# Performance work log

Measured on AMD Instinct MI355X. Metric: run time of the kernel, lower is better.

## Reference

```python
import jax, jax.numpy as jnp
import numpy as np

N_NODES = 50000
N_EDGES = 800000
NODE_DIM = 64
EDGE_DIM = 32
HIDDEN = 128
OUT_DIM = 32
N_LAYERS = 3
NUM_GRAPHS = 128


def setup_inputs() -> dict:
    key = jax.random.key(0)
    ks = jax.random.split(key, 20)
    s = 0.05
    inp = {
        "x": jax.random.normal(ks[0], (N_NODES, NODE_DIM), dtype=jnp.float32),
        "edge_attr": jax.random.normal(ks[1], (N_EDGES, EDGE_DIM), dtype=jnp.float32),
        "edge_index": jax.random.randint(ks[2], (2, N_EDGES), 0, N_NODES, dtype=jnp.int32),
        "batch": jnp.sort(jax.random.randint(ks[3], (N_NODES,), 0, NUM_GRAPHS, dtype=jnp.int32)),
        # per-interaction params, stacked on leading layer axis
        "W_dense": jax.random.normal(ks[4], (N_LAYERS, NODE_DIM, NODE_DIM)) * s,
        "filt_W1": jax.random.normal(ks[5], (N_LAYERS, EDGE_DIM, HIDDEN)) * s,
        "filt_b1": jnp.zeros((N_LAYERS, HIDDEN)),
        "filt_W2": jax.random.normal(ks[6], (N_LAYERS, HIDDEN, NODE_DIM)) * s,
        "filt_b2": jnp.zeros((N_LAYERS, NODE_DIM)),
        "attn_v": jax.random.normal(ks[7], (N_LAYERS, NODE_DIM)) * s,
        "out_W1": jax.random.normal(ks[8], (N_LAYERS, NODE_DIM, HIDDEN)) * s,
        "out_b1": jnp.zeros((N_LAYERS, HIDDEN)),
        "out_W2": jax.random.normal(ks[9], (N_LAYERS, HIDDEN, NODE_DIM)) * s,
        "out_b2": jnp.zeros((N_LAYERS, NODE_DIM)),
        # output network
        "net_W1": jax.random.normal(ks[10], (NODE_DIM, HIDDEN)) * s,
        "net_b1": jnp.zeros((HIDDEN,)),
        "net_W2": jax.random.normal(ks[11], (HIDDEN, OUT_DIM)) * s,
        "net_b2": jnp.zeros((OUT_DIM,)),
    }
    return inp


def _mlp2(x, W1, b1, W2, b2):
    # 2-layer MLP with tanh after first layer (matches MLP(num_layers=2, act='tanh'))
    return jnp.tanh(x @ W1 + b1) @ W2 + b2


def reference(x, edge_attr, W_dense, filt_W1, filt_b1, filt_W2, filt_b2,
              attn_v, out_W1, out_b1, out_W2, out_b2,
              net_W1, net_b1, net_W2, net_b2, edge_index, batch):
    n_nodes = x.shape[0]
    src, tgt = edge_index[0], edge_index[1]
    h = x
    for i in range(N_LAYERS):
        hd = h @ W_dense[i]                                   # initial_dense (no bias)
        edge_w = _mlp2(edge_attr, filt_W1[i], filt_b1[i], filt_W2[i], filt_b2[i])  # [E, D]
        messages = hd[src] * edge_w                           # [E, D]
        # per-target segment softmax over attention scores
        scores = messages @ attn_v[i]                         # [E]
        seg_max = jax.ops.segment_max(scores, tgt, num_segments=n_nodes)
        exp_s = jnp.exp(scores - seg_max[tgt])
        denom = jax.ops.segment_sum(exp_s, tgt, num_segments=n_nodes)
        attn_w = exp_s / denom[tgt]                           # [E]
        messages = messages * attn_w[:, None]
        agg = jax.ops.segment_sum(messages, tgt, num_segments=n_nodes)  # [N, D]
        delta = _mlp2(agg, out_W1[i], out_b1[i], out_W2[i], out_b2[i])
        h = h + delta                                         # residual
    # mean pooling per graph
    pooled = jax.ops.segment_sum(h, batch, num_segments=NUM_GRAPHS)
    counts = jnp.bincount(batch, length=NUM_GRAPHS)
    pooled = pooled / jnp.maximum(counts, 1)[:, None].astype(h.dtype)
    out = _mlp2(pooled, net_W1, net_b1, net_W2, net_b2)       # [G, OUT_DIM]
    return out
```

## Files before the change

### kernel.cpp

```cpp
#include <hip/hip_runtime.h>
#include <hip/hip_bf16.h>
#include <math.h>

#define NODE_DIM 64
#define EDGE_DIM 32
#define HIDDEN   128
#define OUT_DIM  32
#define N_LAYERS 3
#define NGRAPH   128

typedef __attribute__((ext_vector_type(8))) short bf16x8;
typedef __attribute__((ext_vector_type(4))) float f32x4;

__device__ __forceinline__ unsigned short f2bf(float f) {
    unsigned u = __float_as_uint(f);
    u = (u + 0x7fffu + ((u >> 16) & 1u)) >> 16;
    return (unsigned short)u;
}
__device__ __forceinline__ float bf2f(unsigned short h) {
    return __uint_as_float((unsigned)h << 16);
}
__device__ __forceinline__ float fast_tanh(float x) {
    float ax = fabsf(x);
    float e = __expf(-2.f * ax);
    float r = __builtin_amdgcn_rcpf(1.f + e);
    float t = (1.f - e) * r;
    return __builtin_copysignf(t, x);
}

__global__ __launch_bounds__(256) void coarse_hist_kernel(
    const int* __restrict__ tgt, int* __restrict__ Hc, int E, int C, int NB) {
    __shared__ int lh[512];
    int blk = blockIdx.x, tid = threadIdx.x;
    for (int b = tid; b < C; b += 256) lh[b] = 0;
    __syncthreads();
    int base = blk * 4096;
#pragma unroll
    for (int i = 0; i < 16; ++i) {
        int e = base + i * 256 + tid;
        if (e < E) atomicAdd(&lh[tgt[e] >> 7], 1);
    }
    __syncthreads();
    for (int b = tid; b < C; b += 256) Hc[(size_t)b * NB + blk] = lh[b];
}

__global__ __launch_bounds__(256) void scan1_kernel(const int* __restrict__ c,
                                                    int* __restrict__ o,
                                                    int* __restrict__ bsum, int n) {
    __shared__ int sh[256];
    int b = blockIdx.x, t = threadIdx.x;
    int i = b * 256 + t;
    int v = (i < n) ? c[i] : 0;
    sh[t] = v;
    __syncthreads();
    for (int d = 1; d < 256; d <<= 1) {
        int u = (t >= d) ? sh[t - d] : 0;
        __syncthreads();
        sh[t] += u;
        __syncthreads();
    }
    if (i < n) o[i] = sh[t] - v;
    if (t == 255) bsum[b] = sh[255];
}

__global__ void scan2_kernel(int* __restrict__ bsum, int nb) {
    __shared__ int sh[1024];
    int t = threadIdx.x;
    int v = (t < nb) ? bsum[t] : 0;
    sh[t] = v;
    __syncthreads();
    for (int d = 1; d < 1024; d <<= 1) {
        int u = (t >= d) ? sh[t - d] : 0;
        __syncthreads();
        sh[t] += u;
        __syncthreads();
    }
    if (t < nb) bsum[t] = sh[t] - v;
}

__global__ __launch_bounds__(256) void scan3_kernel(int* __restrict__ o,
                                                    const int* __restrict__ bsum, int n) {
    int i = blockIdx.x * 256 + threadIdx.x;
    if (i < n) o[i] += bsum[blockIdx.x];
}

__global__ __launch_bounds__(256) void coarse_scatter_kernel(
    const int* __restrict__ tgt, const int* __restrict__ Sc,
    int* __restrict__ tgtc, int* __restrict__ ec, int E, int C, int NB) {
    __shared__ int lb[512];
    int blk = blockIdx.x, tid = threadIdx.x;
    for (int b = tid; b < C; b += 256) lb[b] = Sc[(size_t)b * NB + blk];
    __syncthreads();
    int base = blk * 4096;
#pragma unroll
    for (int i = 0; i < 16; ++i) {
        int e = base + i * 256 + tid;
        if (e < E) {
            int t = tgt[e];
            int pos = atomicAdd(&lb[t >> 7], 1);
            tgtc[pos] = t;
            ec[pos] = e;
        }
    }
}

__global__ __launch_bounds__(256) void fine_sort_kernel(
    const int* __restrict__ Sc, const int* __restrict__ tgtc,
    const int* __restrict__ ec, const int* __restrict__ src,
    int* __restrict__ off, int* __restrict__ eidx, int* __restrict__ srcp,
    int E, int N, int C, int NB) {
    __shared__ int fh[128], fs[128], rb[128];
    int b = blockIdx.x, tid = threadIdx.x;
    int cb0 = Sc[(size_t)b * NB];
    int cb1 = (b + 1 < C) ? Sc[(size_t)(b + 1) * NB] : E;
    if (tid < 128) fh[tid] = 0;
    __syncthreads();
    for (int p = cb0 + tid; p < cb1; p += 256) atomicAdd(&fh[tgtc[p] & 127], 1);
    __syncthreads();
    if (tid < 128) fs[tid] = fh[tid];
    __syncthreads();
    for (int d = 1; d < 128; d <<= 1) {
        int v = 0;
        if (tid < 128 && tid >= d) v = fs[tid - d];
        __syncthreads();
        if (tid < 128) fs[tid] += v;
        __syncthreads();
    }
    if (tid < 128) {
        int ex = fs[tid] - fh[tid];
        rb[tid] = ex;
        int node = (b << 7) + tid;
        if (node < N) off[node] = cb0 + ex;
    }
    if (b == C - 1 && tid == 0) off[N] = E;
    __syncthreads();
    for (int p = cb0 + tid; p < cb1; p += 256) {
        int t = tgtc[p];
        int r = atomicAdd(&rb[t & 127], 1);
        int fpos = cb0 + r;
        int e = ec[p];
        eidx[fpos] = e;
        srcp[fpos] = src[e];
    }
}

__global__ void gbound_kernel(const int* __restrict__ batch, int* __restrict__ goff,
                              int N, int G) {
    int i = blockIdx.x * 256 + threadIdx.x;
    if (i >= N) return;
    int b = batch[i];
    if (i == 0) {
        for (int g = 0; g <= b; ++g) goff[g] = 0;
    } else {
        int bp = batch[i - 1];
        for (int g = bp + 1; g <= b; ++g) goff[g] = i;
    }
    if (i == N - 1) {
        for (int g = b + 1; g <= G; ++g) goff[g] = N;
    }
}

__global__ __launch_bounds__(256) void perm_ea_kernel(
    const float* __restrict__ ea, const int* __restrict__ eidx,
    unsigned short* __restrict__ out, int E) {
    int p = blockIdx.x * 256 + threadIdx.x;
    if (p >= E) return;
    int e = eidx[p];
    const float4* r = (const float4*)(ea + (size_t)e * EDGE_DIM);
    union { unsigned short us[EDGE_DIM]; uint4 u4[EDGE_DIM / 8]; } tmp;
#pragma unroll
    for (int q = 0; q < EDGE_DIM / 4; ++q) {
        float4 v = r[q];
        tmp.us[4 * q]     = f2bf(v.x);
        tmp.us[4 * q + 1] = f2bf(v.y);
        tmp.us[4 * q + 2] = f2bf(v.z);
        tmp.us[4 * q + 3] = f2bf(v.w);
    }
    uint4* o = (uint4*)(out + (size_t)p * EDGE_DIM);
#pragma unroll
    for (int k = 0; k < EDGE_DIM / 8; ++k) o[k] = tmp.u4[k];
}

__global__ void swizzle_w_kernel(const float* __restrict__ fW1, const float* __restrict__ fW2,
                                 const float* __restrict__ oW1, const float* __restrict__ oW2,
                                 unsigned short* __restrict__ W1sw, unsigned short* __restrict__ W2sw,
                                 unsigned short* __restrict__ oW1sw, unsigned short* __restrict__ oW2sw) {
    int i = blockIdx.x / 56, r = blockIdx.x % 56;
    int L = threadIdx.x;
    int e = L & 15, q = L >> 4;
    const float* W;
    unsigned short* out;
    int K, M, t;
    if (r < 8)       { W = fW1 + (size_t)i * EDGE_DIM * HIDDEN;  out = W1sw  + (size_t)i * 8 * 512;  K = EDGE_DIM; M = HIDDEN;   t = r; }
    else if (r < 24) { W = fW2 + (size_t)i * HIDDEN * NODE_DIM;  out = W2sw  + (size_t)i * 16 * 512; K = HIDDEN;   M = NODE_DIM; t = r - 8; }
    else if (r < 40) { W = oW1 + (size_t)i * NODE_DIM * HIDDEN;  out = oW1sw + (size_t)i * 16 * 512; K = NODE_DIM; M = HIDDEN;   t = r - 24; }
    else             { W = oW2 + (size_t)i * HIDDEN * NODE_DIM;  out = oW2sw + (size_t)i * 16 * 512; K = HIDDEN;   M = NODE_DIM; t = r - 40; }
    int nc = K >> 5;
    int mt = t / nc, s = t - mt * nc;
    union { unsigned short us[8]; uint4 u4; } pk;
#pragma unroll
    for (int j = 0; j < 8; ++j)
        pk.us[j] = f2bf(W[(size_t)(32 * s + 8 * q + j) * M + 16 * mt + e]);
    *(uint4*)(out + ((size_t)t * 64 + L) * 8) = pk.u4;
}

#define HSTRIDE 136

__global__ __launch_bounds__(256) void edge_mfma_kernel(
    const unsigned short* __restrict__ ea_p, const float* __restrict__ hd,
    const unsigned short* __restrict__ W1sw, const float* __restrict__ b1,
    const unsigned short* __restrict__ W2sw, const float* __restrict__ b2,
    const float* __restrict__ av, const int* __restrict__ srcp,
    unsigned short* __restrict__ ew, float* __restrict__ score, int E) {
    __shared__ unsigned short Hl[4][16 * HSTRIDE];
    int wave = threadIdx.x >> 6, lane = threadIdx.x & 63;
    int e = lane & 15, q = lane >> 4;
    int p0 = blockIdx.x * 64 + wave * 16;
    if (p0 >= E) return;

    bf16x8 eaf = *(const bf16x8*)(ea_p + (size_t)(p0 + e) * EDGE_DIM + q * 8);

    f32x4 c1[8];
#pragma unroll
    for (int t = 0; t < 8; ++t) {
        bf16x8 a = *(const bf16x8*)(W1sw + (t * 64 + lane) * 8);
        c1[t] = __builtin_amdgcn_mfma_f32_16x16x32_bf16(a, eaf, (f32x4){0.f, 0.f, 0.f, 0.f}, 0, 0, 0);
    }

    unsigned short* hrow = &Hl[wave][e * HSTRIDE];
#pragma unroll
    for (int t = 0; t < 8; ++t) {
        float4 b = *(const float4*)(b1 + 16 * t + 4 * q);
        unsigned h0 = f2bf(fast_tanh(c1[t][0] + b.x));
        unsigned h1 = f2bf(fast_tanh(c1[t][1] + b.y));
        unsigned h2 = f2bf(fast_tanh(c1[t][2] + b.z));
        unsigned h3 = f2bf(fast_tanh(c1[t][3] + b.w));
        uint2 pk;
        pk.x = h0 | (h1 << 16);
        pk.y = h2 | (h3 << 16);
        *(uint2*)(hrow + 16 * t + 4 * q) = pk;
    }

    f32x4 c2[4] = {{0.f, 0.f, 0.f, 0.f}, {0.f, 0.f, 0.f, 0.f},
                   {0.f, 0.f, 0.f, 0.f}, {0.f, 0.f, 0.f, 0.f}};
#pragma unroll
    for (int s = 0; s < 4; ++s) {
        bf16x8 hf = *(const bf16x8*)(hrow + 32 * s + 8 * q);
#pragma unroll
        for (int nt = 0; nt < 4; ++nt) {
            bf16x8 a = *(const bf16x8*)(W2sw + ((nt * 4 + s) * 64 + lane) * 8);
            c2[nt] = __builtin_amdgcn_mfma_f32_16x16x32_bf16(a, hf, c2[nt], 0, 0, 0);
        }
    }

    int sidx = srcp[p0 + e];
    float sc = 0.f;
#pragma unroll
    for (int nt = 0; nt < 4; ++nt) {
        float4 bb = *(const float4*)(b2 + 16 * nt + 4 * q);
        float4 vv = *(const float4*)(av + 16 * nt + 4 * q);
        float4 hh = *(const float4*)(hd + (size_t)sidx * NODE_DIM + 16 * nt + 4 * q);
        float e0 = c2[nt][0] + bb.x, e1 = c2[nt][1] + bb.y;
        float e2 = c2[nt][2] + bb.z, e3 = c2[nt][3] + bb.w;
        uint2 pk;
        pk.x = (unsigned)f2bf(e0) | ((unsigned)f2bf(e1) << 16);
        pk.y = (unsigned)f2bf(e2) | ((unsigned)f2bf(e3) << 16);
        *(uint2*)(ew + (size_t)(p0 + e) * NODE_DIM + 16 * nt + 4 * q) = pk;
        sc += hh.x * e0 * vv.x + hh.y * e1 * vv.y + hh.z * e2 * vv.z + hh.w * e3 * vv.w;
    }
    sc += __shfl_xor(sc, 16, 64);
    sc += __shfl_xor(sc, 32, 64);
    if (q == 0) score[p0 + e] = sc;
}

__global__ __launch_bounds__(256) void node_mlp_kernel(
    const float* __restrict__ agg,
    const unsigned short* __restrict__ W1sw, const float* __restrict__ b1,
    const unsigned short* __restrict__ W2sw, const float* __restrict__ b2,
    float* __restrict__ h, int N) {
    __shared__ unsigned short Hl[4][16 * HSTRIDE];
    int wave = threadIdx.x >> 6, lane = threadIdx.x & 63;
    int e = lane & 15, q = lane >> 4;
    int n0 = (blockIdx.x * 4 + wave) * 16;
    if (n0 >= N) return;
    int ne = n0 + e;
    int neC = ne < N ? ne : N - 1;
    bool ok = ne < N;

    bf16x8 bfr[2];
#pragma unroll
    for (int s = 0; s < 2; ++s) {
        const float4* ar = (const float4*)(agg + (size_t)neC * NODE_DIM + 32 * s + 8 * q);
        float4 x0 = ar[0], x1 = ar[1];
        union { bf16x8 v; unsigned short us[8]; } u;
        u.us[0] = f2bf(x0.x); u.us[1] = f2bf(x0.y);
        u.us[2] = f2bf(x0.z); u.us[3] = f2bf(x0.w);
        u.us[4] = f2bf(x1.x); u.us[5] = f2bf(x1.y);
        u.us[6] = f2bf(x1.z); u.us[7] = f2bf(x1.w);
        bfr[s] = u.v;
    }

    f32x4 c1[8];
#pragma unroll
    for (int t = 0; t < 8; ++t) {
        bf16x8 a0 = *(const bf16x8*)(W1sw + ((t * 2 + 0) * 64 + lane) * 8);
        bf16x8 a1 = *(const bf16x8*)(W1sw + ((t * 2 + 1) * 64 + lane) * 8);
        c1[t] = __builtin_amdgcn_mfma_f32_16x16x32_bf16(a0, bfr[0], (f32x4){0.f, 0.f, 0.f, 0.f}, 0, 0, 0);
        c1[t] = __builtin_amdgcn_mfma_f32_16x16x32_bf16(a1, bfr[1], c1[t], 0, 0, 0);
    }

    unsigned short* hrow = &Hl[wave][e * HSTRIDE];
#pragma unroll
    for (int t = 0; t < 8; ++t) {
        float4 b = *(const float4*)(b1 + 16 * t + 4 * q);
        unsigned h0 = f2bf(fast_tanh(c1[t][0] + b.x));
        unsigned h1 = f2bf(fast_tanh(c1[t][1] + b.y));
        unsigned h2 = f2bf(fast_tanh(c1[t][2] + b.z));
        unsigned h3 = f2bf(fast_tanh(c1[t][3] + b.w));
        uint2 pk;
        pk.x = h0 | (h1 << 16);
        pk.y = h2 | (h3 << 16);
        *(uint2*)(hrow + 16 * t + 4 * q) = pk;
    }

    f32x4 c2[4] = {{0.f, 0.f, 0.f, 0.f}, {0.f, 0.f, 0.f, 0.f},
                   {0.f, 0.f, 0.f, 0.f}, {0.f, 0.f, 0.f, 0.f}};
#pragma unroll
    for (int s = 0; s < 4; ++s) {
        bf16x8 hf = *(const bf16x8*)(hrow + 32 * s + 8 * q);
#pragma unroll
        for (int nt = 0; nt < 4; ++nt) {
            bf16x8 a = *(const bf16x8*)(W2sw + ((nt * 4 + s) * 64 + lane) * 8);
            c2[nt] = __builtin_amdgcn_mfma_f32_16x16x32_bf16(a, hf, c2[nt], 0, 0, 0);
        }
    }

    if (ok) {
#pragma unroll
        for (int nt = 0; nt < 4; ++nt) {
            float4 bb = *(const float4*)(b2 + 16 * nt + 4 * q);
            float4* hp = (float4*)(h + (size_t)ne * NODE_DIM + 16 * nt + 4 * q);
            float4 hv = *hp;
            hv.x += c2[nt][0] + bb.x;
            hv.y += c2[nt][1] + bb.y;
            hv.z += c2[nt][2] + bb.z;
            hv.w += c2[nt][3] + bb.w;
            *hp = hv;
        }
    }
}

template <int K, int M, bool ACT, bool RESID>
__global__ __launch_bounds__(256) void dense_kernel(
    const float* __restrict__ X, const float* __restrict__ W,
    const float* __restrict__ bias, float* __restrict__ Y, int rows) {
    int tid = blockIdx.x * 256 + threadIdx.x;
    int row = tid / M;
    int d = tid - row * M;
    if (row >= rows) return;
    if (M >= 64) row = __builtin_amdgcn_readfirstlane(row);
    const float* __restrict__ x = X + (size_t)row * K;
    float acc = bias ? bias[d] : 0.f;
#pragma unroll
    for (int k = 0; k < K; ++k) acc += x[k] * W[k * M + d];
    if (ACT) acc = fast_tanh(acc);
    if (RESID) acc += Y[(size_t)row * M + d];
    Y[(size_t)row * M + d] = acc;
}

__global__ __launch_bounds__(256) void agg_kernel(
    const unsigned short* __restrict__ ew, const float* __restrict__ score,
    const float* __restrict__ hd, const int* __restrict__ srcp,
    const int* __restrict__ off, float* __restrict__ agg, int n) {
    int tid = blockIdx.x * 256 + threadIdx.x;
    int wid = tid >> 6;
    int lane = threadIdx.x & 63;
    if (wid >= n) return;
    wid = __builtin_amdgcn_readfirstlane(wid);
    int o0 = off[wid], o1 = off[wid + 1];
    int g = lane >> 3, s = lane & 7;
    if (o1 <= o0) {
        if (g == 0) {
            float4 z = {0.f, 0.f, 0.f, 0.f};
            float4* dst = (float4*)(agg + (size_t)wid * NODE_DIM + s * 8);
            dst[0] = z; dst[1] = z;
        }
        return;
    }
    float m = -INFINITY;
    for (int p = o0 + lane; p < o1; p += 64) m = fmaxf(m, score[p]);
#pragma unroll
    for (int t = 32; t; t >>= 1) m = fmaxf(m, __shfl_xor(m, t, 64));
    float dsum = 0.f;
    for (int p = o0 + lane; p < o1; p += 64) dsum += __expf(score[p] - m);
#pragma unroll
    for (int t = 32; t; t >>= 1) dsum += __shfl_xor(dsum, t, 64);

    float acc[8] = {0.f, 0.f, 0.f, 0.f, 0.f, 0.f, 0.f, 0.f};
    for (int p = o0; p < o1; p += 8) {
        int pe = p + g;
        int pc = (pe < o1) ? pe : (o1 - 1);
        float w = (pe < o1) ? __expf(score[pc] - m) : 0.f;
        int sidx = srcp[pc];
        union { bf16x8 v; unsigned short us[8]; } eu;
        eu.v = *(const bf16x8*)(ew + (size_t)pc * NODE_DIM + s * 8);
        const float4* hr = (const float4*)(hd + (size_t)sidx * NODE_DIM + s * 8);
        float4 h0 = hr[0], h1 = hr[1];
        acc[0] += w * h0.x * bf2f(eu.us[0]);
        acc[1] += w * h0.y * bf2f(eu.us[1]);
        acc[2] += w * h0.z * bf2f(eu.us[2]);
        acc[3] += w * h0.w * bf2f(eu.us[3]);
        acc[4] += w * h1.x * bf2f(eu.us[4]);
        acc[5] += w * h1.y * bf2f(eu.us[5]);
        acc[6] += w * h1.z * bf2f(eu.us[6]);
        acc[7] += w * h1.w * bf2f(eu.us[7]);
    }
#pragma unroll
    for (int j = 0; j < 8; ++j) {
        acc[j] += __shfl_xor(acc[j], 8, 64);
        acc[j] += __shfl_xor(acc[j], 16, 64);
        acc[j] += __shfl_xor(acc[j], 32, 64);
    }
    if (g == 0) {
        float inv = __builtin_amdgcn_rcpf(dsum);
        inv = inv * (2.f - dsum * inv);
        float4 r0 = {acc[0] * inv, acc[1] * inv, acc[2] * inv, acc[3] * inv};
        float4 r1 = {acc[4] * inv, acc[5] * inv, acc[6] * inv, acc[7] * inv};
        float4* dst = (float4*)(agg + (size_t)wid * NODE_DIM + s * 8);
        dst[0] = r0; dst[1] = r1;
    }
}

__global__ __launch_bounds__(256) void pool_kernel(const float* __restrict__ h,
                                                   const int* __restrict__ goff,
                                                   float* __restrict__ pooled) {
    __shared__ float sh[4][NODE_DIM];
    int g = blockIdx.x;
    int w = threadIdx.x >> 6, d = threadIdx.x & 63;
    int o0 = goff[g], o1 = goff[g + 1];
    float acc = 0.f;
    for (int n = o0 + w; n < o1; n += 4) acc += h[(size_t)n * NODE_DIM + d];
    sh[w][d] = acc;
    __syncthreads();
    if (w == 0) {
        float sum = sh[0][d] + sh[1][d] + sh[2][d] + sh[3][d];
        int c = o1 - o0;
        if (c < 1) c = 1;
        pooled[g * NODE_DIM + d] = sum / (float)c;
    }
}

extern "C" void kernel_launch(void* const* d_in, const int* in_sizes, int n_in,
                              void* d_out, int out_size, void* d_ws, size_t ws_size,
                              hipStream_t stream) {
    const float* x         = (const float*)d_in[0];
    const float* edge_attr = (const float*)d_in[1];
    const int*   ei        = (const int*)d_in[2];
    const int*   batch     = (const int*)d_in[3];
    const float* Wd        = (const float*)d_in[4];
    const float* fW1       = (const float*)d_in[5];
    const float* fb1       = (const float*)d_in[6];
    const float* fW2       = (const float*)d_in[7];
    const float* fb2       = (const float*)d_in[8];
    const float* av        = (const float*)d_in[9];
    const float* oW1       = (const float*)d_in[10];
    const float* ob1       = (const float*)d_in[11];
    const float* oW2       = (const float*)d_in[12];
    const float* ob2       = (const float*)d_in[13];
    const float* nW1       = (const float*)d_in[14];
    const float* nb1       = (const float*)d_in[15];
    const float* nW2       = (const float*)d_in[16];
    const float* nb2       = (const float*)d_in[17];
    float* out = (float*)d_out;

    const int N = in_sizes[0] / NODE_DIM;
    const int E = in_sizes[2] / 2;
    const int G = NGRAPH;
    const int NB = (E + 4095) / 4096;
    const int C  = (N + 127) >> 7;
    const int SN = C * NB;
    const int SB = (SN + 255) / 256;

    char* base = (char*)d_ws;
    size_t pos = 0;
    auto alloc = [&](size_t bytes) -> void* {
        pos = (pos + 255) & ~(size_t)255;
        void* r = base + pos;
        pos += bytes;
        return r;
    };
    int* Hc   = (int*)alloc((size_t)SN * 4);
    int* Sc   = (int*)alloc(((size_t)SN + 1) * 4);
    int* bsum = (int*)alloc((size_t)1024 * 4);
    int* tgtc = (int*)alloc((size_t)E * 4);
    int* ec   = (int*)alloc((size_t)E * 4);
    int* off  = (int*)alloc((size_t)(N + 1) * 4);
    int* goff = (int*)alloc((size_t)(G + 1) * 4);
    int* eidx = (int*)alloc((size_t)E * 4);
    int* srcp = (int*)alloc((size_t)E * 4);
    float* score = (float*)alloc((size_t)E * 4);
    float* hd    = (float*)alloc((size_t)N * NODE_DIM * 4);
    float* h     = (float*)alloc((size_t)N * NODE_DIM * 4);
    float* agg   = (float*)alloc((size_t)N * NODE_DIM * 4);
    float* pooled = (float*)alloc((size_t)G * NODE_DIM * 4);
    float* t2     = (float*)alloc((size_t)G * HIDDEN * 4);
    unsigned short* ea_p  = (unsigned short*)alloc((size_t)E * EDGE_DIM * 2);
    unsigned short* ew    = (unsigned short*)alloc((size_t)E * NODE_DIM * 2);
    unsigned short* W1sw  = (unsigned short*)alloc((size_t)N_LAYERS * 8 * 512 * 2);
    unsigned short* W2sw  = (unsigned short*)alloc((size_t)N_LAYERS * 16 * 512 * 2);
    unsigned short* oW1sw = (unsigned short*)alloc((size_t)N_LAYERS * 16 * 512 * 2);
    unsigned short* oW2sw = (unsigned short*)alloc((size_t)N_LAYERS * 16 * 512 * 2);
    (void)ws_size;

    const int* src = ei;
    const int* tgt = ei + E;

    coarse_hist_kernel<<<NB, 256, 0, stream>>>(tgt, Hc, E, C, NB);
    scan1_kernel<<<SB, 256, 0, stream>>>(Hc, Sc, bsum, SN);
    scan2_kernel<<<1, 1024, 0, stream>>>(bsum, SB);
    scan3_kernel<<<SB, 256, 0, stream>>>(Sc, bsum, SN);
    coarse_scatter_kernel<<<NB, 256, 0, stream>>>(tgt, Sc, tgtc, ec, E, C, NB);
    fine_sort_kernel<<<C, 256, 0, stream>>>(Sc, tgtc, ec, src, off, eidx, srcp, E, N, C, NB);
    gbound_kernel<<<(N + 255) / 256, 256, 0, stream>>>(batch, goff, N, G);
    perm_ea_kernel<<<(E + 255) / 256, 256, 0, stream>>>(edge_attr, eidx, ea_p, E);
    swizzle_w_kernel<<<N_LAYERS * 56, 64, 0, stream>>>(fW1, fW2, oW1, oW2, W1sw, W2sw, oW1sw, oW2sw);
    hipMemcpyAsync(h, x, (size_t)N * NODE_DIM * 4, hipMemcpyDeviceToDevice, stream);

    const int node_tiles = (N + 15) / 16;
    for (int i = 0; i < N_LAYERS; ++i) {
        dense_kernel<NODE_DIM, NODE_DIM, false, false>
            <<<(N * NODE_DIM + 255) / 256, 256, 0, stream>>>(
                h, Wd + (size_t)i * NODE_DIM * NODE_DIM, nullptr, hd, N);
        edge_mfma_kernel<<<(E + 63) / 64, 256, 0, stream>>>(
            ea_p, hd,
            W1sw + (size_t)i * 8 * 512, fb1 + (size_t)i * HIDDEN,
            W2sw + (size_t)i * 16 * 512, fb2 + (size_t)i * NODE_DIM,
            av + (size_t)i * NODE_DIM, srcp, ew, score, E);
        agg_kernel<<<(N + 3) / 4, 256, 0, stream>>>(ew, score, hd, srcp, off, agg, N);
        node_mlp_kernel<<<(node_tiles + 3) / 4, 256, 0, stream>>>(
            agg,
            oW1sw + (size_t)i * 16 * 512, ob1 + (size_t)i * HIDDEN,
            oW2sw + (size_t)i * 16 * 512, ob2 + (size_t)i * NODE_DIM,
            h, N);
    }

    pool_kernel<<<G, 256, 0, stream>>>(h, goff, pooled);
    dense_kernel<NODE_DIM, HIDDEN, true, false>
        <<<(G * HIDDEN + 255) / 256, 256, 0, stream>>>(pooled, nW1, nb1, t2, G);
    dense_kernel<HIDDEN, OUT_DIM, false, false>
        <<<(G * OUT_DIM + 255) / 256, 256, 0, stream>>>(t2, nW2, nb2, out, G);
}
```

Measured before the change: 853.8 us.

## Fuse edge filter MLP, softmax aggregation and node MLP into one per-node-block kernel

Replaces the separate edge MLP, aggregation and node MLP kernels with one kernel. Each block owns 64 target nodes, computes the filter MLP for their CSR-sorted edges, accumulates exp-weighted messages into shared memory with LDS atomics, then runs the output MLP and residual update in place. This removes the global round trips for the bf16 edge weights, the scores and the agg buffer. The softmax no longer subtracts a per-segment max and instead clamps scores at 60, which could lose precision. Load balance now depends on per-block edge counts, and the LDS atomics may contend.

```diff
diff --git a/kernel.cpp b/kernel.cpp
--- a/kernel.cpp
+++ b/kernel.cpp
@@ -108,7 +108,7 @@
     const int* __restrict__ Sc, const int* __restrict__ tgtc,
     const int* __restrict__ ec, const int* __restrict__ src,
     int* __restrict__ off, int* __restrict__ eidx, int* __restrict__ srcp,
-    int E, int N, int C, int NB) {
+    int* __restrict__ tgts, int E, int N, int C, int NB) {
     __shared__ int fh[128], fs[128], rb[128];
     int b = blockIdx.x, tid = threadIdx.x;
     int cb0 = Sc[(size_t)b * NB];
@@ -141,6 +141,7 @@
         int e = ec[p];
         eidx[fpos] = e;
         srcp[fpos] = src[e];
+        tgts[fpos] = t;
     }
 }
 
@@ -205,147 +206,177 @@
 }
 
 #define HSTRIDE 136
-
-__global__ __launch_bounds__(256) void edge_mfma_kernel(
+#define NG 64
+
+__global__ __launch_bounds__(256, 4) void edge_agg_kernel(
     const unsigned short* __restrict__ ea_p, const float* __restrict__ hd,
     const unsigned short* __restrict__ W1sw, const float* __restrict__ b1,
     const unsigned short* __restrict__ W2sw, const float* __restrict__ b2,
     const float* __restrict__ av, const int* __restrict__ srcp,
-    unsigned short* __restrict__ ew, float* __restrict__ score, int E) {
-    __shared__ unsigned short Hl[4][16 * HSTRIDE];
-    int wave = threadIdx.x >> 6, lane = threadIdx.x & 63;
+    const int* __restrict__ tgts, const int* __restrict__ off,
+    const unsigned short* __restrict__ oW1sw, const float* __restrict__ ob1,
+    const unsigned short* __restrict__ oW2sw, const float* __restrict__ ob2,
+    float* __restrict__ h, int N) {
+    __shared__ float scr[4][16 * 68];
+    __shared__ float acc[NG * 65];
+    __shared__ float den[NG];
+
+    int tid = threadIdx.x;
+    int wave = tid >> 6, lane = tid & 63;
     int e = lane & 15, q = lane >> 4;
-    int p0 = blockIdx.x * 64 + wave * 16;
-    if (p0 >= E) return;
-
-    bf16x8 eaf = *(const bf16x8*)(ea_p + (size_t)(p0 + e) * EDGE_DIM + q * 8);
-
-    f32x4 c1[8];
+    int n0 = blockIdx.x * NG;
+    int n1 = n0 + NG; if (n1 > N) n1 = N;
+    int e0 = off[n0], e1 = off[n1];
+
+    for (int i = tid; i < NG * 65; i += 256) acc[i] = 0.f;
+    if (tid < NG) den[tid] = 0.f;
+    __syncthreads();
+
+    float* swrow = &scr[wave][0];
+    unsigned short* hrow = (unsigned short*)swrow + e * HSTRIDE;
+
+    int nch = (e1 - e0 + 63) >> 6;
+    for (int c = 0; c < nch; ++c) {
+        int p0 = e0 + c * 64 + wave * 16;
+        if (p0 < e1) {
+            int pe = p0 + e;
+            int pc = pe < e1 ? pe : e1 - 1;
+            bool valid = pe < e1;
+
+            bf16x8 eaf = *(const bf16x8*)(ea_p + (size_t)pc * EDGE_DIM + q * 8);
+            f32x4 c1[8];
+#pragma unroll
+            for (int t = 0; t < 8; ++t) {
+                bf16x8 a = *(const bf16x8*)(W1sw + (t * 64 + lane) * 8);
+                c1[t] = __builtin_amdgcn_mfma_f32_16x16x32_bf16(a, eaf, (f32x4){0.f, 0.f, 0.f, 0.f}, 0, 0, 0);
+            }
+#pragma unroll
+            for (int t = 0; t < 8; ++t) {
+                float4 bb = *(const float4*)(b1 + 16 * t + 4 * q);
+                unsigned h0 = f2bf(fast_tanh(c1[t][0] + bb.x));
+                unsigned h1 = f2bf(fast_tanh(c1[t][1] + bb.y));
+                unsigned h2 = f2bf(fast_tanh(c1[t][2] + bb.z));
+                unsigned h3 = f2bf(fast_tanh(c1[t][3] + bb.w));
+                uint2 pk;
+                pk.x = h0 | (h1 << 16);
+                pk.y = h2 | (h3 << 16);
+                *(uint2*)(hrow + 16 * t + 4 * q) = pk;
+            }
+
+            f32x4 c2[4] = {{0.f, 0.f, 0.f, 0.f}, {0.f, 0.f, 0.f, 0.f},
+                           {0.f, 0.f, 0.f, 0.f}, {0.f, 0.f, 0.f, 0.f}};
+#pragma unroll
+            for (int s = 0; s < 4; ++s) {
+                bf16x8 hf = *(const bf16x8*)(hrow + 32 * s + 8 * q);
+#pragma unroll
+                for (int nt = 0; nt < 4; ++nt) {
+                    bf16x8 a = *(const bf16x8*)(W2sw + ((nt * 4 + s) * 64 + lane) * 8);
+                    c2[nt] = __builtin_amdgcn_mfma_f32_16x16x32_bf16(a, hf, c2[nt], 0, 0, 0);
+                }
+            }
+
+            int sidx = srcp[pc];
+            int tg = tgts[pc] - n0;
+            float4 hv[4];
+            float sc = 0.f;
+#pragma unroll
+            for (int nt = 0; nt < 4; ++nt) {
+                float4 bb = *(const float4*)(b2 + 16 * nt + 4 * q);
+                float4 vv = *(const float4*)(av + 16 * nt + 4 * q);
+                float4 hh = *(const float4*)(hd + (size_t)sidx * NODE_DIM + 16 * nt + 4 * q);
+                c2[nt][0] += bb.x; c2[nt][1] += bb.y;
+                c2[nt][2] += bb.z; c2[nt][3] += bb.w;
+                hv[nt] = hh;
+                sc += hh.x * c2[nt][0] * vv.x + hh.y * c2[nt][1] * vv.y
+                    + hh.z * c2[nt][2] * vv.z + hh.w * c2[nt][3] * vv.w;
+            }
+            sc += __shfl_xor(sc, 16, 64);
+            sc += __shfl_xor(sc, 32, 64);
+            float w = valid ? __expf(fminf(sc, 60.f)) : 0.f;
+
+#pragma unroll
+            for (int nt = 0; nt < 4; ++nt) {
+                f32x4 cv;
+                cv[0] = w * hv[nt].x * c2[nt][0];
+                cv[1] = w * hv[nt].y * c2[nt][1];
+                cv[2] = w * hv[nt].z * c2[nt][2];
+                cv[3] = w * hv[nt].w * c2[nt][3];
+                *(f32x4*)(swrow + e * 68 + 16 * nt + 4 * q) = cv;
+            }
+            if (q == 0) {
+                swrow[e * 68 + 67] = __int_as_float(tg);
+                atomicAdd(&den[tg], w);
+            }
+#pragma unroll
+            for (int e2 = 0; e2 < 16; ++e2) {
+                int tg2 = __float_as_int(swrow[e2 * 68 + 67]);
+                float cv = swrow[e2 * 68 + lane];
+                atomicAdd(&acc[tg2 * 65 + lane], cv);
+            }
+        }
+    }
+    __syncthreads();
+
+    int nl = wave * 16 + e;
+    int ne = n0 + nl;
+    bool ok = ne < N;
+    float dv = den[nl];
+    float inv = __builtin_amdgcn_rcpf(dv);
+    inv = inv * (2.f - dv * inv);
+    if (!(dv > 0.f)) inv = 0.f;
+
+    bf16x8 bfr[2];
+#pragma unroll
+    for (int s = 0; s < 2; ++s) {
+        union { bf16x8 v; unsigned short us[8]; } u;
+#pragma unroll
+        for (int j = 0; j < 8; ++j)
+            u.us[j] = f2bf(acc[nl * 65 + 32 * s + 8 * q + j] * inv);
+        bfr[s] = u.v;
+    }
+
+    f32x4 d1[8];
 #pragma unroll
     for (int t = 0; t < 8; ++t) {
-        bf16x8 a = *(const bf16x8*)(W1sw + (t * 64 + lane) * 8);
-        c1[t] = __builtin_amdgcn_mfma_f32_16x16x32_bf16(a, eaf, (f32x4){0.f, 0.f, 0.f, 0.f}, 0, 0, 0);
-    }
-
-    unsigned short* hrow = &Hl[wave][e * HSTRIDE];
+        bf16x8 a0 = *(const bf16x8*)(oW1sw + ((t * 2 + 0) * 64 + lane) * 8);
+        bf16x8 a1 = *(const bf16x8*)(oW1sw + ((t * 2 + 1) * 64 + lane) * 8);
+        d1[t] = __builtin_amdgcn_mfma_f32_16x16x32_bf16(a0, bfr[0], (f32x4){0.f, 0.f, 0.f, 0.f}, 0, 0, 0);
+        d1[t] = __builtin_amdgcn_mfma_f32_16x16x32_bf16(a1, bfr[1], d1[t], 0, 0, 0);
+    }
 #pragma unroll
     for (int t = 0; t < 8; ++t) {
-        float4 b = *(const float4*)(b1 + 16 * t + 4 * q);
-        unsigned h0 = f2bf(fast_tanh(c1[t][0] + b.x));
-        unsigned h1 = f2bf(fast_tanh(c1[t][1] + b.y));
-        unsigned h2 = f2bf(fast_tanh(c1[t][2] + b.z));
-        unsigned h3 = f2bf(fast_tanh(c1[t][3] + b.w));
+        float4 bb = *(const float4*)(ob1 + 16 * t + 4 * q);
+        unsigned h0 = f2bf(fast_tanh(d1[t][0] + bb.x));
+        unsigned h1 = f2bf(fast_tanh(d1[t][1] + bb.y));
+        unsigned h2 = f2bf(fast_tanh(d1[t][2] + bb.z));
+        unsigned h3 = f2bf(fast_tanh(d1[t][3] + bb.w));
         uint2 pk;
         pk.x = h0 | (h1 << 16);
         pk.y = h2 | (h3 << 16);
         *(uint2*)(hrow + 16 * t + 4 * q) = pk;
     }
-
-    f32x4 c2[4] = {{0.f, 0.f, 0.f, 0.f}, {0.f, 0.f, 0.f, 0.f},
+    f32x4 d2[4] = {{0.f, 0.f, 0.f, 0.f}, {0.f, 0.f, 0.f, 0.f},
                    {0.f, 0.f, 0.f, 0.f}, {0.f, 0.f, 0.f, 0.f}};
 #pragma unroll
     for (int s = 0; s < 4; ++s) {
         bf16x8 hf = *(const bf16x8*)(hrow + 32 * s + 8 * q);
 #pragma unroll
         for (int nt = 0; nt < 4; ++nt) {
-            bf16x8 a = *(const bf16x8*)(W2sw + ((nt * 4 + s) * 64 + lane) * 8);
-            c2[nt] = __builtin_amdgcn_mfma_f32_16x16x32_bf16(a, hf, c2[nt], 0, 0, 0);
+            bf16x8 a = *(const bf16x8*)(oW2sw + ((nt * 4 + s) * 64 + lane) * 8);
+            d2[nt] = __builtin_amdgcn_mfma_f32_16x16x32_bf16(a, hf, d2[nt], 0, 0, 0);
         }
     }
-
-    int sidx = srcp[p0 + e];
-    float sc = 0.f;
-#pragma unroll
-    for (int nt = 0; nt < 4; ++nt) {
-        float4 bb = *(const float4*)(b2 + 16 * nt + 4 * q);
-        float4 vv = *(const float4*)(av + 16 * nt + 4 * q);
-        float4 hh = *(const float4*)(hd + (size_t)sidx * NODE_DIM + 16 * nt + 4 * q);
-        float e0 = c2[nt][0] + bb.x, e1 = c2[nt][1] + bb.y;
-        float e2 = c2[nt][2] + bb.z, e3 = c2[nt][3] + bb.w;
-        uint2 pk;
-        pk.x = (unsigned)f2bf(e0) | ((unsigned)f2bf(e1) << 16);
-        pk.y = (unsigned)f2bf(e2) | ((unsigned)f2bf(e3) << 16);
-        *(uint2*)(ew + (size_t)(p0 + e) * NODE_DIM + 16 * nt + 4 * q) = pk;
-        sc += hh.x * e0 * vv.x + hh.y * e1 * vv.y + hh.z * e2 * vv.z + hh.w * e3 * vv.w;
-    }
-    sc += __shfl_xor(sc, 16, 64);
-    sc += __shfl_xor(sc, 32, 64);
-    if (q == 0) score[p0 + e] = sc;
-}
-
-__global__ __launch_bounds__(256) void node_mlp_kernel(
-    const float* __restrict__ agg,
-    const unsigned short* __restrict__ W1sw, const float* __restrict__ b1,
-    const unsigned short* __restrict__ W2sw, const float* __restrict__ b2,
-    float* __restrict__ h, int N) {
-    __shared__ unsigned short Hl[4][16 * HSTRIDE];
-    int wave = threadIdx.x >> 6, lane = threadIdx.x & 63;
-    int e = lane & 15, q = lane >> 4;
-    int n0 = (blockIdx.x * 4 + wave) * 16;
-    if (n0 >= N) return;
-    int ne = n0 + e;
-    int neC = ne < N ? ne : N - 1;
-    bool ok = ne < N;
-
-    bf16x8 bfr[2];
-#pragma unroll
-    for (int s = 0; s < 2; ++s) {
-        const float4* ar = (const float4*)(agg + (size_t)neC * NODE_DIM + 32 * s + 8 * q);
-        float4 x0 = ar[0], x1 = ar[1];
-        union { bf16x8 v; unsigned short us[8]; } u;
-        u.us[0] = f2bf(x0.x); u.us[1] = f2bf(x0.y);
-        u.us[2] = f2bf(x0.z); u.us[3] = f2bf(x0.w);
-        u.us[4] = f2bf(x1.x); u.us[5] = f2bf(x1.y);
-        u.us[6] = f2bf(x1.z); u.us[7] = f2bf(x1.w);
-        bfr[s] = u.v;
-    }
-
-    f32x4 c1[8];
-#pragma unroll
-    for (int t = 0; t < 8; ++t) {
-        bf16x8 a0 = *(const bf16x8*)(W1sw + ((t * 2 + 0) * 64 + lane) * 8);
-        bf16x8 a1 = *(const bf16x8*)(W1sw + ((t * 2 + 1) * 64 + lane) * 8);
-        c1[t] = __builtin_amdgcn_mfma_f32_16x16x32_bf16(a0, bfr[0], (f32x4){0.f, 0.f, 0.f, 0.f}, 0, 0, 0);
-        c1[t] = __builtin_amdgcn_mfma_f32_16x16x32_bf16(a1, bfr[1], c1[t], 0, 0, 0);
-    }
-
-    unsigned short* hrow = &Hl[wave][e * HSTRIDE];
-#pragma unroll
-    for (int t = 0; t < 8; ++t) {
-        float4 b = *(const float4*)(b1 + 16 * t + 4 * q);
-        unsigned h0 = f2bf(fast_tanh(c1[t][0] + b.x));
-        unsigned h1 = f2bf(fast_tanh(c1[t][1] + b.y));
-        unsigned h2 = f2bf(fast_tanh(c1[t][2] + b.z));
-        unsigned h3 = f2bf(fast_tanh(c1[t][3] + b.w));
-        uint2 pk;
-        pk.x = h0 | (h1 << 16);
-        pk.y = h2 | (h3 << 16);
-        *(uint2*)(hrow + 16 * t + 4 * q) = pk;
-    }
-
-    f32x4 c2[4] = {{0.f, 0.f, 0.f, 0.f}, {0.f, 0.f, 0.f, 0.f},
-                   {0.f, 0.f, 0.f, 0.f}, {0.f, 0.f, 0.f, 0.f}};
-#pragma unroll
-    for (int s = 0; s < 4; ++s) {
-        bf16x8 hf = *(const bf16x8*)(hrow + 32 * s + 8 * q);
+    if (ok) {
 #pragma unroll
         for (int nt = 0; nt < 4; ++nt) {
-            bf16x8 a = *(const bf16x8*)(W2sw + ((nt * 4 + s) * 64 + lane) * 8);
-            c2[nt] = __builtin_amdgcn_mfma_f32_16x16x32_bf16(a, hf, c2[nt], 0, 0, 0);
-        }
-    }
-
-    if (ok) {
-#pragma unroll
-        for (int nt = 0; nt < 4; ++nt) {
-            float4 bb = *(const float4*)(b2 + 16 * nt + 4 * q);
+            float4 bb = *(const float4*)(ob2 + 16 * nt + 4 * q);
             float4* hp = (float4*)(h + (size_t)ne * NODE_DIM + 16 * nt + 4 * q);
-            float4 hv = *hp;
-            hv.x += c2[nt][0] + bb.x;
-            hv.y += c2[nt][1] + bb.y;
-            hv.z += c2[nt][2] + bb.z;
-            hv.w += c2[nt][3] + bb.w;
-            *hp = hv;
+            float4 hvv = *hp;
+            hvv.x += d2[nt][0] + bb.x;
+            hvv.y += d2[nt][1] + bb.y;
+            hvv.z += d2[nt][2] + bb.z;
+            hvv.w += d2[nt][3] + bb.w;
+            *hp = hvv;
         }
     }
 }
@@ -366,69 +397,6 @@
     if (ACT) acc = fast_tanh(acc);
     if (RESID) acc += Y[(size_t)row * M + d];
     Y[(size_t)row * M + d] = acc;
-}
-
-__global__ __launch_bounds__(256) void agg_kernel(
-    const unsigned short* __restrict__ ew, const float* __restrict__ score,
-    const float* __restrict__ hd, const int* __restrict__ srcp,
-    const int* __restrict__ off, float* __restrict__ agg, int n) {
-    int tid = blockIdx.x * 256 + threadIdx.x;
-    int wid = tid >> 6;
-    int lane = threadIdx.x & 63;
-    if (wid >= n) return;
-    wid = __builtin_amdgcn_readfirstlane(wid);
-    int o0 = off[wid], o1 = off[wid + 1];
-    int g = lane >> 3, s = lane & 7;
-    if (o1 <= o0) {
-        if (g == 0) {
-            float4 z = {0.f, 0.f, 0.f, 0.f};
-            float4* dst = (float4*)(agg + (size_t)wid * NODE_DIM + s * 8);
-            dst[0] = z; dst[1] = z;
-        }
-        return;
-    }
-    float m = -INFINITY;
-    for (int p = o0 + lane; p < o1; p += 64) m = fmaxf(m, score[p]);
-#pragma unroll
-    for (int t = 32; t; t >>= 1) m = fmaxf(m, __shfl_xor(m, t, 64));
-    float dsum = 0.f;
-    for (int p = o0 + lane; p < o1; p += 64) dsum += __expf(score[p] - m);
-#pragma unroll
-    for (int t = 32; t; t >>= 1) dsum += __shfl_xor(dsum, t, 64);
-
-    float acc[8] = {0.f, 0.f, 0.f, 0.f, 0.f, 0.f, 0.f, 0.f};
-    for (int p = o0; p < o1; p += 8) {
-        int pe = p + g;
-        int pc = (pe < o1) ? pe : (o1 - 1);
-        float w = (pe < o1) ? __expf(score[pc] - m) : 0.f;
-        int sidx = srcp[pc];
-        union { bf16x8 v; unsigned short us[8]; } eu;
-        eu.v = *(const bf16x8*)(ew + (size_t)pc * NODE_DIM + s * 8);
-        const float4* hr = (const float4*)(hd + (size_t)sidx * NODE_DIM + s * 8);
-        float4 h0 = hr[0], h1 = hr[1];
-        acc[0] += w * h0.x * bf2f(eu.us[0]);
-        acc[1] += w * h0.y * bf2f(eu.us[1]);
-        acc[2] += w * h0.z * bf2f(eu.us[2]);
-        acc[3] += w * h0.w * bf2f(eu.us[3]);
-        acc[4] += w * h1.x * bf2f(eu.us[4]);
-        acc[5] += w * h1.y * bf2f(eu.us[5]);
-        acc[6] += w * h1.z * bf2f(eu.us[6]);
-        acc[7] += w * h1.w * bf2f(eu.us[7]);
-    }
-#pragma unroll
-    for (int j = 0; j < 8; ++j) {
-        acc[j] += __shfl_xor(acc[j], 8, 64);
-        acc[j] += __shfl_xor(acc[j], 16, 64);
-        acc[j] += __shfl_xor(acc[j], 32, 64);
-    }
-    if (g == 0) {
-        float inv = __builtin_amdgcn_rcpf(dsum);
-        inv = inv * (2.f - dsum * inv);
-        float4 r0 = {acc[0] * inv, acc[1] * inv, acc[2] * inv, acc[3] * inv};
-        float4 r1 = {acc[4] * inv, acc[5] * inv, acc[6] * inv, acc[7] * inv};
-        float4* dst = (float4*)(agg + (size_t)wid * NODE_DIM + s * 8);
-        dst[0] = r0; dst[1] = r1;
-    }
 }
 
 __global__ __launch_bounds__(256) void pool_kernel(const float* __restrict__ h,
@@ -498,14 +466,12 @@
     int* goff = (int*)alloc((size_t)(G + 1) * 4);
     int* eidx = (int*)alloc((size_t)E * 4);
     int* srcp = (int*)alloc((size_t)E * 4);
-    float* score = (float*)alloc((size_t)E * 4);
+    int* tgts = (int*)alloc((size_t)E * 4);
     float* hd    = (float*)alloc((size_t)N * NODE_DIM * 4);
     float* h     = (float*)alloc((size_t)N * NODE_DIM * 4);
-    float* agg   = (float*)alloc((size_t)N * NODE_DIM * 4);
     float* pooled = (float*)alloc((size_t)G * NODE_DIM * 4);
     float* t2     = (float*)alloc((size_t)G * HIDDEN * 4);
     unsigned short* ea_p  = (unsigned short*)alloc((size_t)E * EDGE_DIM * 2);
-    unsigned short* ew    = (unsigned short*)alloc((size_t)E * NODE_DIM * 2);
     unsigned short* W1sw  = (unsigned short*)alloc((size_t)N_LAYERS * 8 * 512 * 2);
     unsigned short* W2sw  = (unsigned short*)alloc((size_t)N_LAYERS * 16 * 512 * 2);
     unsigned short* oW1sw = (unsigned short*)alloc((size_t)N_LAYERS * 16 * 512 * 2);
@@ -520,25 +486,22 @@
     scan2_kernel<<<1, 1024, 0, stream>>>(bsum, SB);
     scan3_kernel<<<SB, 256, 0, stream>>>(Sc, bsum, SN);
     coarse_scatter_kernel<<<NB, 256, 0, stream>>>(tgt, Sc, tgtc, ec, E, C, NB);
-    fine_sort_kernel<<<C, 256, 0, stream>>>(Sc, tgtc, ec, src, off, eidx, srcp, E, N, C, NB);
+    fine_sort_kernel<<<C, 256, 0, stream>>>(Sc, tgtc, ec, src, off, eidx, srcp, tgts, E, N, C, NB);
     gbound_kernel<<<(N + 255) / 256, 256, 0, stream>>>(batch, goff, N, G);
     perm_ea_kernel<<<(E + 255) / 256, 256, 0, stream>>>(edge_attr, eidx, ea_p, E);
     swizzle_w_kernel<<<N_LAYERS * 56, 64, 0, stream>>>(fW1, fW2, oW1, oW2, W1sw, W2sw, oW1sw, oW2sw);
     hipMemcpyAsync(h, x, (size_t)N * NODE_DIM * 4, hipMemcpyDeviceToDevice, stream);
 
-    const int node_tiles = (N + 15) / 16;
+    const int nblk = (N + NG - 1) / NG;
     for (int i = 0; i < N_LAYERS; ++i) {
         dense_kernel<NODE_DIM, NODE_DIM, false, false>
             <<<(N * NODE_DIM + 255) / 256, 256, 0, stream>>>(
                 h, Wd + (size_t)i * NODE_DIM * NODE_DIM, nullptr, hd, N);
-        edge_mfma_kernel<<<(E + 63) / 64, 256, 0, stream>>>(
+        edge_agg_kernel<<<nblk, 256, 0, stream>>>(
             ea_p, hd,
             W1sw + (size_t)i * 8 * 512, fb1 + (size_t)i * HIDDEN,
             W2sw + (size_t)i * 16 * 512, fb2 + (size_t)i * NODE_DIM,
-            av + (size_t)i * NODE_DIM, srcp, ew, score, E);
-        agg_kernel<<<(N + 3) / 4, 256, 0, stream>>>(ew, score, hd, srcp, off, agg, N);
-        node_mlp_kernel<<<(node_tiles + 3) / 4, 256, 0, stream>>>(
-            agg,
+            av + (size_t)i * NODE_DIM, srcp, tgts, off,
             oW1sw + (size_t)i * 16 * 512, ob1 + (size_t)i * HIDDEN,
             oW2sw + (size_t)i * 16 * 512, ob2 + (size_t)i * NODE_DIM,
             h, N);
```

After: 1.578 ms. 1.85x slower.
